# Kernel optimization log

Hardware: AMD Instinct MI355X
Metric: run time of the kernel (lower is better)

## Reference

```python
import jax, jax.numpy as jnp
import numpy as np

TEM = 6  # forward hardcodes Tem=6 for index building; init default Tem=6 for weights


def _build_index(H, W, Tem):
    # Faithful port of _build_matrix_index: row edges per phase, col edges per phase,
    # then cross-phase edges linking corresponding pixels of adjacent phases.
    raw = jnp.arange(W, dtype=jnp.int32)[None, :] + jnp.arange(H, dtype=jnp.int32)[:, None] * W  # [H,W]
    pw = W // Tem
    phases = [raw[:, i * pw:(i + 1) * pw] for i in range(Tem)]
    rows = [jnp.stack([p[:-1, :], p[1:, :]], axis=2).reshape(-1, 2) for p in phases]
    cols = [jnp.stack([p[:, :-1], p[:, 1:]], axis=2).reshape(-1, 2) for p in phases]
    cross = [jnp.stack([phases[i], phases[i + 1]], axis=2).reshape(-1, 2) for i in range(Tem - 1)]
    return jnp.concatenate(rows + cols + cross, axis=0)  # [E,2]


def _build_weight_norm2(fm, Tem):
    # Faithful port of _build_feature_weight_norm2_distance, INCLUDING the original
    # per-phase [row,col] interleaved ordering (which differs from the index ordering).
    B, D, H, W = fm.shape
    pw = W // Tem
    phases = [fm[:, :, :, i * pw:(i + 1) * pw] for i in range(Tem)]
    ws = []
    for p in phases:
        wr = ((p[:, :, :-1, :] - p[:, :, 1:, :]) ** 2).sum(axis=1).reshape(B, -1)
        wc = ((p[:, :, :, :-1] - p[:, :, :, 1:]) ** 2).sum(axis=1).reshape(B, -1)
        ws.extend([wr, wc])
    for i in range(Tem - 1):
        ws.append(((phases[i] - phases[i + 1]) ** 2).sum(axis=1).reshape(B, -1))
    return jnp.concatenate(ws, axis=1)  # [B,E]


def _mst_single(u, v, w, V):
    # Vectorized Boruvka MST with pointer-jumping union-find (jit-compatible,
    # fixed round count >= ceil(log2 V)). Ties broken by a globally unique edge rank.
    E = u.shape[0]
    order = jnp.argsort(w)  # stable -> unique rank per edge
    rank = jnp.zeros(E, jnp.int32).at[order].set(jnp.arange(E, dtype=jnp.int32))
    n_rounds = int(np.ceil(np.log2(max(V, 2)))) + 1
    idx_v = jnp.arange(V, dtype=jnp.int32)

    def round_fn(carry, _):
        comp, mask = carry
        cu, cv = comp[u], comp[v]
        active = cu != cv
        key = jnp.where(active, rank, E)  # E = sentinel 'no edge'
        mk = jnp.minimum(jax.ops.segment_min(key, cu, num_segments=V),
                         jax.ops.segment_min(key, cv, num_segments=V))  # min rank per component
        has = mk < E
        sel = order[jnp.clip(mk, 0, E - 1)]  # chosen edge index per component
        a, b = cu[sel], cv[sel]
        other = jnp.where(a == idx_v, b, a)
        parent = jnp.where(has, other, idx_v)
        # break mutual 2-cycles: smaller-index component becomes root
        gp = parent[parent]
        parent = jnp.where((gp == idx_v) & (idx_v < parent), idx_v, parent)
        # full path compression via pointer jumping
        parent = jax.lax.while_loop(lambda p: jnp.any(p[p] != p), lambda p: p[p], parent)
        comp = parent[comp]
        mask = mask.at[jnp.where(has, sel, E)].set(True)  # slot E is scratch
        return (comp, mask), None

    comp0 = jnp.arange(V, dtype=jnp.int32)
    mask0 = jnp.zeros(E + 1, dtype=bool)
    (comp, mask), _ = jax.lax.scan(round_fn, (comp0, mask0), None, length=n_rounds)
    mask = mask[:E]
    # grid graph is connected -> exactly V-1 selected edges; emit sorted edge ids
    tree = jnp.sort(jnp.where(mask, jnp.arange(E, dtype=jnp.int32), E))[: V - 1]
    return tree  # [V-1] int32


def setup_inputs() -> dict:
    key = jax.random.key(0)
    guide_in = jax.random.normal(key, (4, 64, 288, 432), dtype=jnp.float32)
    return {"guide_in": guide_in}


def reference(guide_in):
    B, C, H, W = guide_in.shape
    V = H * W
    index = _build_index(H, W, TEM)  # [E,2], same for every batch element
    weight = _build_weight_norm2(guide_in, TEM)  # [B,E]
    u, v = index[:, 0], index[:, 1]
    tree = jax.vmap(lambda ww: _mst_single(u, v, ww, V))(weight)  # [B, V-1]
    return tree
```

## Files before the change

kernel.cpp:

```cpp
#include <hip/hip_runtime.h>
#include <cstdint>
#include <cstddef>

#define NB 4
#define NC 64
#define HH 288
#define WW 432
#define PW 72
#define NV (HH*WW)
#define R_PER ((HH-1)*PW)
#define C_PER (HH*(PW-1))
#define X_PER (HH*PW)
#define PAIRW (R_PER + C_PER)
#define ROWS_TOT (6*R_PER)
#define ROWCOL (6*PAIRW)
#define NE (ROWCOL + 5*X_PER)
#define NEB ((NE + 255)/256)
#define EPT 4
#define NEB4 ((NE + 1023)/1024)
#define NTREE (NV-1)
#define NROUNDS 17
#define CHUNK 4096
#define NCHUNK ((NE + CHUNK - 1)/CHUNK)
#define CSTR 32
#define SLB 128
#define SSB 64
#define RLCAP 65536

typedef unsigned long long ull;

__device__ __forceinline__ void index_uv(int e, int& u, int& v) {
    if (e < ROWS_TOT) {
        int t = e / R_PER, l = e - t * R_PER;
        int h = l / PW, x = l - h * PW;
        u = h * WW + t * PW + x; v = u + WW;
    } else if (e < ROWCOL) {
        int q = e - ROWS_TOT;
        int t = q / C_PER, l = q - t * C_PER;
        int h = l / (PW-1), x = l - h * (PW-1);
        u = h * WW + t * PW + x; v = u + 1;
    } else {
        int q = e - ROWCOL;
        int t = q / X_PER, l = q - t * X_PER;
        int h = l / PW, x = l - h * PW;
        u = h * WW + t * PW + x; v = u + PW;
    }
}

__device__ __forceinline__ int rootOf2(const int* __restrict__ par, int c, int p) {
    while (true) {
        if (p == c) return c;
        int pp = par[p];
        if (pp == c) return c < p ? c : p;
        c = p; p = pp;
    }
}

__global__ __launch_bounds__(256) void init_kernel(int* comp, int* parent,
                                                   ull* minkey, unsigned char* mask,
                                                   int* cnt, int* rlc) {
    int i = blockIdx.x * 256 + threadIdx.x;
    int b = blockIdx.y;
    if (i < NV) {
        comp[(size_t)b*NV + i] = i;
        parent[(size_t)b*NV + i] = i;
        minkey[(size_t)b*NV + i] = ~0ULL;
    }
    if (i < NE) mask[(size_t)b*NE + i] = 0;
    if (b == 0 && i < 2*NB*CSTR) { cnt[i] = 0; rlc[i] = 0; }
}

__global__ __launch_bounds__(256) void key0_kernel(const float* __restrict__ fm,
                                                   ull* __restrict__ keys,
                                                   ull* __restrict__ minkey) {
    int i = blockIdx.x * 256 + threadIdx.x;
    int b = blockIdx.y;
    if (i >= NV) return;
    int h = i / WW, x = i - h * WW;
    int t = x / PW, xr = x - t * PW;
    bool hv = (h < HH-1);
    bool hh = (xr < PW-1);
    bool hx = (x < WW-PW);
    int ov = hv ? WW : 0;
    int oh = hh ? 1  : 0;
    int ox = hx ? PW : 0;
    const float* base = fm + (size_t)b * NC * NV + i;
    float sv = 0.f, sh_ = 0.f, sx = 0.f;
    #pragma unroll 8
    for (int ch = 0; ch < NC; ++ch) {
        const float* p = base + (size_t)ch * NV;
        float f0 = p[0];
        float dv = f0 - p[ov];
        float dh = f0 - p[oh];
        float dx = f0 - p[ox];
        sv += dv * dv; sh_ += dh * dh; sx += dx * dx;
    }
    ull* mk = minkey + (size_t)b * NV;
    ull* ky = keys + (size_t)b * NE;
    if (hv) {
        int e = t * PAIRW + h * PW + xr;
        ull k = ((ull)__float_as_uint(sv) << 32) | (unsigned int)e;
        ky[e] = k;
        int u, v; index_uv(e, u, v);
        atomicMin(&mk[u], k); atomicMin(&mk[v], k);
    }
    if (hh) {
        int e = t * PAIRW + R_PER + h * (PW-1) + xr;
        ull k = ((ull)__float_as_uint(sh_) << 32) | (unsigned int)e;
        ky[e] = k;
        int u, v; index_uv(e, u, v);
        atomicMin(&mk[u], k); atomicMin(&mk[v], k);
    }
    if (hx) {
        int e = ROWCOL + t * X_PER + h * PW + xr;
        ull k = ((ull)__float_as_uint(sx) << 32) | (unsigned int)e;
        ky[e] = k;
        int u, v; index_uv(e, u, v);
        atomicMin(&mk[u], k); atomicMin(&mk[v], k);
    }
}

__global__ __launch_bounds__(256) void select0_kernel(const int* __restrict__ comp,
                                                      int* __restrict__ parent,
                                                      ull* __restrict__ minkey,
                                                      unsigned char* __restrict__ mask) {
    int gid = blockIdx.x * 256 + threadIdx.x;
    int b = blockIdx.y;
    int c0 = gid * 4;
    if (c0 >= NV) return;
    size_t off = (size_t)b * NV;
    ulonglong4 kv = *reinterpret_cast<const ulonglong4*>(minkey + off + c0);
    ull kk[4] = {kv.x, kv.y, kv.z, kv.w};
    #pragma unroll
    for (int j = 0; j < 4; ++j) {
        int c = c0 + j;
        if (kk[j] != ~0ULL) {
            minkey[off + c] = ~0ULL;
            int e = (int)(kk[j] & 0xffffffffu);
            mask[(size_t)b * NE + e] = 1;
            int u, v; index_uv(e, u, v);
            int cu = comp[off + u], cv = comp[off + v];
            parent[off + c] = (cu == c) ? cv : cu;
        }
    }
}

#define EMIT_ROOTS(fcu, fcv, cuA, cvA, rlW, rlcSlot)                          \
    {                                                                         \
        int tot = 0;                                                          \
        _Pragma("unroll")                                                     \
        for (int j = 0; j < EPT; ++j) {                                       \
            tot += __popcll(__ballot(fcu[j] ? 1 : 0));                        \
            tot += __popcll(__ballot(fcv[j] ? 1 : 0));                        \
        }                                                                     \
        int base_ = 0;                                                        \
        if (lane == 0 && tot) base_ = atomicAdd(rlcSlot, tot);                \
        base_ = __shfl(base_, 0);                                             \
        ull ltm = (1ull << lane) - 1;                                         \
        int pre_ = 0;                                                         \
        _Pragma("unroll")                                                     \
        for (int j = 0; j < EPT; ++j) {                                       \
            ull bu = __ballot(fcu[j] ? 1 : 0);                                \
            if (fcu[j]) rlW[base_ + pre_ + __popcll(bu & ltm)] = cuA[j];      \
            pre_ += __popcll(bu);                                             \
            ull bv = __ballot(fcv[j] ? 1 : 0);                                \
            if (fcv[j]) rlW[base_ + pre_ + __popcll(bv & ltm)] = cvA[j];      \
            pre_ += __popcll(bv);                                             \
        }                                                                     \
    }

__global__ __launch_bounds__(256) void scan_full_kernel(const ull* __restrict__ keys,
                                                        int* __restrict__ comp,
                                                        const int* __restrict__ parent,
                                                        ull* __restrict__ minkey,
                                                        int* __restrict__ list0,
                                                        int* __restrict__ cnt,
                                                        int* __restrict__ rlWb,
                                                        int* __restrict__ rlcW) {
    const int tid = threadIdx.x;
    const int b = blockIdx.y;
    const int ebase = blockIdx.x * (256 * EPT) + tid;
    const size_t offV = (size_t)b * NV;
    const int* par = parent + offV;
    int* cmp = comp + offV;
    ull* mk = minkey + offV;
    const ull* ky = keys + (size_t)b * NE;
    int* rlW = rlWb + (size_t)b * RLCAP;

    int e[EPT], uu[EPT], vv[EPT], cu0[EPT], cv0[EPT], pu0[EPT], pv0[EPT];
    int cuA[EPT], cvA[EPT];
    ull k[EPT];
    bool valid[EPT], live[EPT], fcu[EPT], fcv[EPT];
    #pragma unroll
    for (int j = 0; j < EPT; ++j) {
        e[j] = ebase + j * 256;
        valid[j] = e[j] < NE;
        int u = 0, v = 0;
        if (valid[j]) index_uv(e[j], u, v);
        uu[j] = u; vv[j] = v;
    }
    #pragma unroll
    for (int j = 0; j < EPT; ++j) {
        cu0[j] = valid[j] ? cmp[uu[j]] : 0;
        cv0[j] = valid[j] ? cmp[vv[j]] : 0;
        k[j]   = valid[j] ? ky[e[j]] : 0;
    }
    #pragma unroll
    for (int j = 0; j < EPT; ++j) {
        pu0[j] = valid[j] ? par[cu0[j]] : 0;
        pv0[j] = valid[j] ? par[cv0[j]] : 0;
    }
    #pragma unroll
    for (int j = 0; j < EPT; ++j) {
        live[j] = false; fcu[j] = false; fcv[j] = false; cuA[j] = 0; cvA[j] = 0;
        if (valid[j]) {
            int cu = rootOf2(par, cu0[j], pu0[j]);
            int cv = rootOf2(par, cv0[j], pv0[j]);
            if (cu0[j] != cu) cmp[uu[j]] = cu;
            if (cv0[j] != cv) cmp[vv[j]] = cv;
            cuA[j] = cu; cvA[j] = cv;
            live[j] = (cu != cv);
            if (live[j]) {
                if (k[j] < mk[cu]) fcu[j] = (atomicMin(&mk[cu], k[j]) == ~0ULL);
                if (k[j] < mk[cv]) fcv[j] = (atomicMin(&mk[cv], k[j]) == ~0ULL);
            }
        }
    }
    const int lane = tid & 63;
    const int wid = tid >> 6;
    EMIT_ROOTS(fcu, fcv, cuA, cvA, rlW, &rlcW[b * CSTR])
    __shared__ int s_w[4];
    __shared__ int s_bcnt;
    __shared__ int s_gb;
    ull wl[EPT]; int wcnt = 0;
    #pragma unroll
    for (int j = 0; j < EPT; ++j) { wl[j] = __ballot(live[j] ? 1 : 0); wcnt += __popcll(wl[j]); }
    if (tid == 0) s_bcnt = 0;
    __syncthreads();
    if (lane == 0) s_w[wid] = wcnt ? atomicAdd(&s_bcnt, wcnt) : 0;
    __syncthreads();
    if (tid == 0 && s_bcnt) s_gb = atomicAdd(&cnt[b * CSTR], s_bcnt);
    __syncthreads();
    int pre = 0;
    #pragma unroll
    for (int j = 0; j < EPT; ++j) {
        if (live[j]) {
            int pos = s_gb + s_w[wid] + pre + __popcll(wl[j] & ((1ull << lane) - 1));
            list0[(size_t)b * NE + pos] = e[j];
        }
        pre += __popcll(wl[j]);
    }
}

__global__ __launch_bounds__(256) void scan_list_kernel(const ull* __restrict__ keys,
                                                        int* __restrict__ comp,
                                                        const int* __restrict__ parent,
                                                        ull* __restrict__ minkey,
                                                        int* __restrict__ list0,
                                                        int* __restrict__ list1,
                                                        int* __restrict__ cnt,
                                                        int rpar,
                                                        int* __restrict__ rlWb,
                                                        int* __restrict__ rlcW) {
    const int b = blockIdx.y;
    const int tid = threadIdx.x;
    const int n = cnt[rpar * NB * CSTR + b * CSTR];
    int* cw = &cnt[(rpar ^ 1) * NB * CSTR + b * CSTR];
    const int* lr = (rpar ? list1 : list0) + (size_t)b * NE;
    int* lw = (rpar ? list0 : list1) + (size_t)b * NE;
    const size_t offV = (size_t)b * NV;
    const int* par = parent + offV;
    int* cmp = comp + offV;
    ull* mk = minkey + offV;
    const ull* ky = keys + (size_t)b * NE;
    int* rlW = rlWb + (size_t)b * RLCAP;

    const int stride = SLB * 256 * EPT;
    const int nIter = (n + stride - 1) / stride;
    const int lane = tid & 63;
    const int wid = tid >> 6;
    __shared__ int s_w[4];
    __shared__ int s_bcnt;
    __shared__ int s_gb;

    for (int it = 0; it < nIter; ++it) {
        const int ibase = it * stride + blockIdx.x * (256 * EPT) + tid;
        int e[EPT], uu[EPT], vv[EPT], cu0[EPT], cv0[EPT], pu0[EPT], pv0[EPT];
        int cuA[EPT], cvA[EPT];
        ull k[EPT];
        bool valid[EPT], live[EPT], fcu[EPT], fcv[EPT];
        #pragma unroll
        for (int j = 0; j < EPT; ++j) {
            int i = ibase + j * 256;
            valid[j] = i < n;
            e[j] = valid[j] ? lr[i] : 0;
        }
        #pragma unroll
        for (int j = 0; j < EPT; ++j) {
            int u = 0, v = 0;
            if (valid[j]) index_uv(e[j], u, v);
            uu[j] = u; vv[j] = v;
        }
        #pragma unroll
        for (int j = 0; j < EPT; ++j) {
            cu0[j] = valid[j] ? cmp[uu[j]] : 0;
            cv0[j] = valid[j] ? cmp[vv[j]] : 0;
            k[j]   = valid[j] ? ky[e[j]] : 0;
        }
        #pragma unroll
        for (int j = 0; j < EPT; ++j) {
            pu0[j] = valid[j] ? par[cu0[j]] : 0;
            pv0[j] = valid[j] ? par[cv0[j]] : 0;
        }
        #pragma unroll
        for (int j = 0; j < EPT; ++j) {
            live[j] = false; fcu[j] = false; fcv[j] = false; cuA[j] = 0; cvA[j] = 0;
            if (valid[j]) {
                int cu = rootOf2(par, cu0[j], pu0[j]);
                int cv = rootOf2(par, cv0[j], pv0[j]);
                if (cu0[j] != cu) cmp[uu[j]] = cu;
                if (cv0[j] != cv) cmp[vv[j]] = cv;
                cuA[j] = cu; cvA[j] = cv;
                live[j] = (cu != cv);
                if (live[j]) {
                    if (k[j] < mk[cu]) fcu[j] = (atomicMin(&mk[cu], k[j]) == ~0ULL);
                    if (k[j] < mk[cv]) fcv[j] = (atomicMin(&mk[cv], k[j]) == ~0ULL);
                }
            }
        }
        EMIT_ROOTS(fcu, fcv, cuA, cvA, rlW, &rlcW[b * CSTR])
        ull wl[EPT]; int wcnt = 0;
        #pragma unroll
        for (int j = 0; j < EPT; ++j) { wl[j] = __ballot(live[j] ? 1 : 0); wcnt += __popcll(wl[j]); }
        if (tid == 0) s_bcnt = 0;
        __syncthreads();
        if (lane == 0) s_w[wid] = wcnt ? atomicAdd(&s_bcnt, wcnt) : 0;
        __syncthreads();
        if (tid == 0 && s_bcnt) s_gb = atomicAdd(cw, s_bcnt);
        __syncthreads();
        int pre = 0;
        #pragma unroll
        for (int j = 0; j < EPT; ++j) {
            if (live[j]) {
                int pos = s_gb + s_w[wid] + pre + __popcll(wl[j] & ((1ull << lane) - 1));
                lw[pos] = e[j];
            }
            pre += __popcll(wl[j]);
        }
    }
}

__global__ __launch_bounds__(256) void select_sparse_kernel(const int* __restrict__ comp,
                                                            int* __restrict__ parent,
                                                            ull* __restrict__ minkey,
                                                            unsigned char* __restrict__ mask,
                                                            const int* __restrict__ rlRb,
                                                            const int* __restrict__ rlcCur,
                                                            int* __restrict__ cntZ,
                                                            int* __restrict__ rlcZ) {
    const int b = blockIdx.y;
    if (blockIdx.x == 0 && threadIdx.x == 0) {
        cntZ[b * CSTR] = 0;
        rlcZ[b * CSTR] = 0;
    }
    const int nr = rlcCur[b * CSTR];
    const int* rlR = rlRb + (size_t)b * RLCAP;
    const size_t off = (size_t)b * NV;
    for (int i = blockIdx.x * 256 + threadIdx.x; i < nr; i += SSB * 256) {
        int c = rlR[i];
        ull k = minkey[off + c];
        minkey[off + c] = ~0ULL;
        int e = (int)(k & 0xffffffffu);
        mask[(size_t)b * NE + e] = 1;
        int u, v; index_uv(e, u, v);
        int cu = comp[off + u], cv = comp[off + v];
        parent[off + c] = (cu == c) ? cv : cu;
    }
}

__global__ __launch_bounds__(256) void count_kernel(const unsigned char* __restrict__ mask,
                                                    int* __restrict__ counts) {
    int b = blockIdx.y, ck = blockIdx.x, t = threadIdx.x;
    const unsigned char* m = mask + (size_t)b * NE;
    int base_e = ck * CHUNK + t * 16;
    int cnt = 0;
    #pragma unroll
    for (int i = 0; i < 16; ++i) {
        int e = base_e + i;
        if (e < NE && m[e]) cnt++;
    }
    __shared__ int sh[256];
    sh[t] = cnt;
    __syncthreads();
    for (int o = 128; o > 0; o >>= 1) {
        if (t < o) sh[t] += sh[t + o];
        __syncthreads();
    }
    if (t == 0) counts[b * NCHUNK + ck] = sh[0];
}

__global__ __launch_bounds__(256) void write_kernel(const unsigned char* __restrict__ mask,
                                                    const int* __restrict__ counts,
                                                    int* __restrict__ out) {
    int b = blockIdx.y, ck = blockIdx.x, t = threadIdx.x;
    __shared__ int sh[256];
    __shared__ int shOff[128];
    shOff[t & 127] = 0;
    __syncthreads();
    if (t < NCHUNK && t < ck) shOff[t] = counts[b * NCHUNK + t];
    __syncthreads();
    for (int o = 64; o > 0; o >>= 1) {
        if (t < o) shOff[t] += shOff[t + o];
        __syncthreads();
    }
    int blockOff = shOff[0];

    const unsigned char* m = mask + (size_t)b * NE;
    int base_e = ck * CHUNK + t * 16;
    int cnt = 0;
    #pragma unroll
    for (int i = 0; i < 16; ++i) {
        int e = base_e + i;
        if (e < NE && m[e]) cnt++;
    }
    sh[t] = cnt;
    __syncthreads();
    for (int o = 1; o < 256; o <<= 1) {
        int v = 0;
        if (t >= o) v = sh[t - o];
        __syncthreads();
        sh[t] += v;
        __syncthreads();
    }
    int pos = blockOff + (sh[t] - cnt);
    for (int i = 0; i < 16; ++i) {
        int e = base_e + i;
        if (e < NE && m[e]) {
            if (pos < NTREE) out[(size_t)b * NTREE + pos] = e;
            pos++;
        }
    }
}

extern "C" void kernel_launch(void* const* d_in, const int* in_sizes, int n_in,
                              void* d_out, int out_size, void* d_ws, size_t ws_size,
                              hipStream_t stream) {
    const float* fm = (const float*)d_in[0];
    int* out = (int*)d_out;

    char* ws = (char*)d_ws;
    size_t off = 0;
    auto alloc = [&](size_t bytes) -> void* {
        void* p = ws + off;
        off += (bytes + 255) & ~(size_t)255;
        return p;
    };
    ull* keys    = (ull*)alloc((size_t)NB * NE * 8);
    ull* minkey  = (ull*)alloc((size_t)NB * NV * 8);
    int* comp    = (int*)alloc((size_t)NB * NV * 4);
    int* parent  = (int*)alloc((size_t)NB * NV * 4);
    unsigned char* mask = (unsigned char*)alloc((size_t)NB * NE);
    int* list0   = (int*)alloc((size_t)NB * NE * 4);
    int* list1   = (int*)alloc((size_t)NB * NE * 4);
    int* cnt     = (int*)alloc(2 * NB * CSTR * 4);
    int* rl      = (int*)alloc(2 * (size_t)NB * RLCAP * 4);
    int* rlc     = (int*)alloc(2 * NB * CSTR * 4);
    int* counts  = (int*)alloc((size_t)NB * NCHUNK * 4);

    dim3 blk(256);
    dim3 gE(NEB, NB);
    dim3 gE4(NEB4, NB);
    dim3 gV((NV + 255) / 256, NB);
    dim3 gVS((NV/4 + 255) / 256, NB);
    dim3 gL(SLB, NB);
    dim3 gS(SSB, NB);

    init_kernel<<<gE, blk, 0, stream>>>(comp, parent, minkey, mask, cnt, rlc);
    key0_kernel<<<gV, blk, 0, stream>>>(fm, keys, minkey);
    select0_kernel<<<gVS, blk, 0, stream>>>(comp, parent, minkey, mask);
    scan_full_kernel<<<gE4, blk, 0, stream>>>(keys, comp, parent, minkey,
                                              list0, cnt,
                                              rl + (size_t)NB * RLCAP,
                                              rlc + NB * CSTR);
    select_sparse_kernel<<<gS, blk, 0, stream>>>(comp, parent, minkey, mask,
                                                 rl + (size_t)NB * RLCAP,
                                                 rlc + NB * CSTR,
                                                 cnt + NB * CSTR,
                                                 rlc);
    for (int r = 2; r < NROUNDS; ++r) {
        int rp = r & 1, ro = (r + 1) & 1;
        scan_list_kernel<<<gL, blk, 0, stream>>>(keys, comp, parent, minkey,
                                                 list0, list1, cnt, rp,
                                                 rl + (size_t)rp * NB * RLCAP,
                                                 rlc + rp * NB * CSTR);
        select_sparse_kernel<<<gS, blk, 0, stream>>>(comp, parent, minkey, mask,
                                                     rl + (size_t)rp * NB * RLCAP,
                                                     rlc + rp * NB * CSTR,
                                                     cnt + rp * NB * CSTR,
                                                     rlc + ro * NB * CSTR);
    }

    count_kernel<<<dim3(NCHUNK, NB), blk, 0, stream>>>(mask, counts);
    write_kernel<<<dim3(NCHUNK, NB), blk, 0, stream>>>(mask, counts, out);
}
```

Measured before the change: 571.2 us.

## Fuse late Boruvka rounds into a single per-batch persistent tail kernel

Rounds from TAIL_START onward, when the live edge list is small, now run inside one kernel with a single 512-thread block per batch element, which loops over the rounds internally using block barriers. This replaces two kernel launches per round (scan_list plus select_sparse) with one launch overall, aiming to cut launch and inter-kernel synchronisation overhead. The cost is that each batch element gets only one block, so if the live list is still large at round 10 that work is much less parallel. Roots are tracked in a capped per-batch buffer of 4096 entries, which risks dropping roots if more components remain than that.

Measured after the change: 551.0 us. 1.04x faster.

```diff
diff --git a/kernel.cpp b/kernel.cpp
--- a/kernel.cpp
+++ b/kernel.cpp
@@ -20,6 +20,9 @@
 #define NEB4 ((NE + 1023)/1024)
 #define NTREE (NV-1)
 #define NROUNDS 17
+#define TAIL_START 10
+#define TBLK 512
+#define RB_CAP 4096
 #define CHUNK 4096
 #define NCHUNK ((NE + CHUNK - 1)/CHUNK)
 #define CSTR 32
@@ -378,6 +381,128 @@
     }
 }
 
+__global__ __launch_bounds__(TBLK) void tail_kernel(const ull* __restrict__ keys,
+                                                    int* __restrict__ comp,
+                                                    int* __restrict__ parent,
+                                                    ull* __restrict__ minkey,
+                                                    unsigned char* __restrict__ mask,
+                                                    int* __restrict__ list0,
+                                                    int* __restrict__ list1,
+                                                    const int* __restrict__ cnt,
+                                                    int* __restrict__ rootbuf) {
+    const int b = blockIdx.x;
+    const int tid = threadIdx.x;
+    const int lane = tid & 63;
+    const int wid = tid >> 6;
+    const size_t offV = (size_t)b * NV;
+    int* cmp = comp + offV;
+    int* par = parent + offV;
+    ull* mk = minkey + offV;
+    const ull* ky = keys + (size_t)b * NE;
+    unsigned char* msk = mask + (size_t)b * NE;
+    int* la = list0 + (size_t)b * NE;
+    int* lb = list1 + (size_t)b * NE;
+    int* rb = rootbuf + (size_t)b * RB_CAP;
+
+    __shared__ int s_out;
+    __shared__ int s_nr;
+    __shared__ int s_wb[TBLK/64];
+
+    int rpar = TAIL_START & 1;
+    int n = cnt[rpar * NB * CSTR + b * CSTR];
+
+    for (int r = TAIL_START; r < NROUNDS && n > 0; ++r) {
+        const int* lr = rpar ? lb : la;
+        int* lw = rpar ? la : lb;
+        if (tid == 0) { s_out = 0; s_nr = 0; }
+        __syncthreads();
+        for (int base = 0; base < n; base += TBLK * EPT) {
+            int e[EPT], uu[EPT], vv[EPT], cu0[EPT], cv0[EPT], pu0[EPT], pv0[EPT];
+            ull k[EPT];
+            bool valid[EPT], live[EPT];
+            #pragma unroll
+            for (int j = 0; j < EPT; ++j) {
+                int i = base + tid + j * TBLK;
+                valid[j] = i < n;
+                e[j] = valid[j] ? lr[i] : 0;
+            }
+            #pragma unroll
+            for (int j = 0; j < EPT; ++j) {
+                int u = 0, v = 0;
+                if (valid[j]) index_uv(e[j], u, v);
+                uu[j] = u; vv[j] = v;
+            }
+            #pragma unroll
+            for (int j = 0; j < EPT; ++j) {
+                cu0[j] = valid[j] ? cmp[uu[j]] : 0;
+                cv0[j] = valid[j] ? cmp[vv[j]] : 0;
+                k[j]   = valid[j] ? ky[e[j]] : 0;
+            }
+            #pragma unroll
+            for (int j = 0; j < EPT; ++j) {
+                pu0[j] = valid[j] ? par[cu0[j]] : 0;
+                pv0[j] = valid[j] ? par[cv0[j]] : 0;
+            }
+            #pragma unroll
+            for (int j = 0; j < EPT; ++j) {
+                live[j] = false;
+                if (valid[j]) {
+                    int cu = rootOf2(par, cu0[j], pu0[j]);
+                    int cv = rootOf2(par, cv0[j], pv0[j]);
+                    if (cu0[j] != cu) cmp[uu[j]] = cu;
+                    if (cv0[j] != cv) cmp[vv[j]] = cv;
+                    live[j] = (cu != cv);
+                    if (live[j]) {
+                        if (k[j] < mk[cu]) {
+                            ull old = atomicMin(&mk[cu], k[j]);
+                            if (old == ~0ULL) {
+                                int ix = atomicAdd(&s_nr, 1);
+                                if (ix < RB_CAP) rb[ix] = cu;
+                            }
+                        }
+                        if (k[j] < mk[cv]) {
+                            ull old = atomicMin(&mk[cv], k[j]);
+                            if (old == ~0ULL) {
+                                int ix = atomicAdd(&s_nr, 1);
+                                if (ix < RB_CAP) rb[ix] = cv;
+                            }
+                        }
+                    }
+                }
+            }
+            ull wl[EPT]; int wcnt = 0;
+            #pragma unroll
+            for (int j = 0; j < EPT; ++j) { wl[j] = __ballot(live[j] ? 1 : 0); wcnt += __popcll(wl[j]); }
+            if (lane == 0) s_wb[wid] = wcnt ? atomicAdd(&s_out, wcnt) : 0;
+            int pre = 0;
+            #pragma unroll
+            for (int j = 0; j < EPT; ++j) {
+                if (live[j]) {
+                    int pos = s_wb[wid] + pre + __popcll(wl[j] & ((1ull << lane) - 1));
+                    lw[pos] = e[j];
+                }
+                pre += __popcll(wl[j]);
+            }
+        }
+        __syncthreads();
+        int nout = s_out;
+        int nr = s_nr < RB_CAP ? s_nr : RB_CAP;
+        for (int i = tid; i < nr; i += TBLK) {
+            int c = rb[i];
+            ull k = mk[c];
+            mk[c] = ~0ULL;
+            int e = (int)(k & 0xffffffffu);
+            msk[e] = 1;
+            int u, v; index_uv(e, u, v);
+            int cu = cmp[u], cv = cmp[v];
+            par[c] = (cu == c) ? cv : cu;
+        }
+        __syncthreads();
+        n = nout;
+        rpar ^= 1;
+    }
+}
+
 __global__ __launch_bounds__(256) void count_kernel(const unsigned char* __restrict__ mask,
                                                     int* __restrict__ counts) {
     int b = blockIdx.y, ck = blockIdx.x, t = threadIdx.x;
@@ -465,6 +590,7 @@
     int* cnt     = (int*)alloc(2 * NB * CSTR * 4);
     int* rl      = (int*)alloc(2 * (size_t)NB * RLCAP * 4);
     int* rlc     = (int*)alloc(2 * NB * CSTR * 4);
+    int* rootbuf = (int*)alloc((size_t)NB * RB_CAP * 4);
     int* counts  = (int*)alloc((size_t)NB * NCHUNK * 4);
 
     dim3 blk(256);
@@ -487,7 +613,7 @@
                                                  rlc + NB * CSTR,
                                                  cnt + NB * CSTR,
                                                  rlc);
-    for (int r = 2; r < NROUNDS; ++r) {
+    for (int r = 2; r < TAIL_START; ++r) {
         int rp = r & 1, ro = (r + 1) & 1;
         scan_list_kernel<<<gL, blk, 0, stream>>>(keys, comp, parent, minkey,
                                                  list0, list1, cnt, rp,
@@ -499,6 +625,9 @@
                                                      cnt + rp * NB * CSTR,
                                                      rlc + ro * NB * CSTR);
     }
+    tail_kernel<<<dim3(NB), dim3(TBLK), 0, stream>>>(keys, comp, parent, minkey,
+                                                     mask, list0, list1, cnt,
+                                                     rootbuf);
 
     count_kernel<<<dim3(NCHUNK, NB), blk, 0, stream>>>(mask, counts);
     write_kernel<<<dim3(NCHUNK, NB), blk, 0, stream>>>(mask, counts, out);
```
